# Optimization experiments

Hardware: AMD Instinct MI355X
Metric: run time of the kernel (lower is better)

## Reference

```python
import jax, jax.numpy as jnp
import numpy as np

DIM = 192
N_HEADS = 8
HEAD_DIM = DIM // N_HEADS
SCALE = 1.0 / np.sqrt(HEAD_DIM).astype(np.float32)
H_GRID, W_GRID = 32, 64
KH, KW = 7, 11


def build_local_mask():
    # Equivalent to the torch double-loop construction: token (h2,w2) may attend
    # to (h,w) iff |h2-h| <= KH//2 and |w2-w| <= KW//2 (odd kernels).
    hh = jnp.arange(H_GRID)
    ww = jnp.arange(W_GRID)
    dh_ok = jnp.abs(hh[:, None] - hh[None, :]) <= KH // 2  # [H, H]
    dw_ok = jnp.abs(ww[:, None] - ww[None, :]) <= KW // 2  # [W, W]
    allowed = dh_ok[:, None, :, None] & dw_ok[None, :, None, :]  # [H, W, H, W]
    allowed = allowed.reshape(H_GRID * W_GRID, H_GRID * W_GRID)
    return jnp.where(allowed, 0.0, -jnp.inf).astype(jnp.float32)  # [N, N]


def setup_inputs() -> dict:
    key = jax.random.key(0)
    ks = jax.random.split(key, 5)
    B, N = 4, H_GRID * W_GRID
    w_std = 1.0 / np.sqrt(DIM)
    x = jax.random.normal(ks[0], (B, N, DIM), dtype=jnp.float32)
    qkv_w = jax.random.normal(ks[1], (3 * DIM, DIM), dtype=jnp.float32) * w_std
    qkv_b = jax.random.normal(ks[2], (3 * DIM,), dtype=jnp.float32) * 0.02
    proj_w = jax.random.normal(ks[3], (DIM, DIM), dtype=jnp.float32) * w_std
    proj_b = jax.random.normal(ks[4], (DIM,), dtype=jnp.float32) * 0.02
    mask = build_local_mask()
    return {"x": x, "qkv_w": qkv_w, "qkv_b": qkv_b,
            "proj_w": proj_w, "proj_b": proj_b, "mask": mask}


def reference(x, qkv_w, qkv_b, proj_w, proj_b, mask):
    B, N, _ = x.shape
    qkv = x @ qkv_w.T + qkv_b                              # [B, N, 3*DIM]
    qkv = qkv.reshape(B, N, 3, N_HEADS, HEAD_DIM)
    qkv = jnp.transpose(qkv, (2, 0, 3, 1, 4))              # [3, B, h, N, d]
    q, k, v = qkv[0] * SCALE, qkv[1], qkv[2]
    attn = jnp.einsum('bhnd,bhmd->bhnm', q, k) + mask      # [B, h, N, N]
    attn = jax.nn.softmax(attn, axis=-1)                   # == log_softmax().exp()
    out = jnp.einsum('bhnm,bhmd->bhnd', attn, v)           # [B, h, N, d]
    out = jnp.transpose(out, (0, 2, 1, 3)).reshape(B, N, DIM)
    return out @ proj_w.T + proj_b
```

## Files before the change

### kernel.cpp

```cpp
#include <hip/hip_runtime.h>
#include <math.h>

#define H_GRID 32
#define W_GRID 64
#define NTOK   2048
#define NHEADS 8
#define HD     24
#define DIMC   192
#define BATCH  4

static constexpr float SCALE = 0.20412414523193154f;

typedef unsigned short ushort;
typedef unsigned int   uint;
typedef __attribute__((ext_vector_type(8))) _Float16 f16x8;
typedef __attribute__((ext_vector_type(4))) float    f32x4;

static __device__ __forceinline__ float4 ld4(const float* p) { return *(const float4*)p; }

static __device__ __forceinline__ ushort f2h(float f) {
    _Float16 h = (_Float16)f;
    union { _Float16 h; ushort u; } c; c.h = h; return c.u;
}
static __device__ __forceinline__ float h2f(ushort u) {
    union { ushort u; _Float16 h; } c; c.u = u; return (float)c.h;
}
static __device__ __forceinline__ f16x8 cvt8(float4 a, float4 b) {
    f16x8 r;
    r[0] = (_Float16)a.x; r[1] = (_Float16)a.y; r[2] = (_Float16)a.z; r[3] = (_Float16)a.w;
    r[4] = (_Float16)b.x; r[5] = (_Float16)b.y; r[6] = (_Float16)b.z; r[7] = (_Float16)b.w;
    return r;
}

__global__ __launch_bounds__(256, 4) void gemm_qkv(const float* __restrict__ x,
                                                   const float* __restrict__ Wf,
                                                   const float* __restrict__ bias,
                                                   ushort* __restrict__ Qh,
                                                   ushort* __restrict__ Kh,
                                                   ushort* __restrict__ VTh) {
    __shared__ ushort Ws[64 * 200];

    const int t    = threadIdx.x;
    const int wave = t >> 6, lane = t & 63;
    const int bx   = blockIdx.x;
    const int by   = blockIdx.y;
    const int m0   = bx * 64 + wave * 16;
    const int j0   = by * 64;
    const int n16  = lane & 15;
    const int kq   = lane >> 4;

    for (int i = t; i < 1536; i += 256) {
        const int r = i / 24, c = i - (i / 24) * 24;
        const float* wsrc = &Wf[(size_t)(j0 + r) * 192 + c * 8];
        const float4 w0 = ld4(wsrc), w1 = ld4(wsrc + 4);
        *(ushort4*)&Ws[r * 200 + c * 8] =
            make_ushort4(f2h(w0.x), f2h(w0.y), f2h(w0.z), f2h(w0.w));
        *(ushort4*)&Ws[r * 200 + c * 8 + 4] =
            make_ushort4(f2h(w1.x), f2h(w1.y), f2h(w1.z), f2h(w1.w));
    }

    if (by == 0) {
        for (int i = t; i < 1024; i += 256) {
            const int tok = bx * 64 + (i >> 4);
            const int h_  = (i >> 1) & 7;
            ushort* dst = (i & 1) ? Kh : Qh;
            const uint4 z = {0u, 0u, 0u, 0u};
            *(uint4*)&dst[((size_t)((tok >> 11) * 8 + h_) * 2048 + (tok & 2047)) * 32 + 24] = z;
        }
    }

    const float* ap = x + (size_t)(m0 + n16) * 192 + kq * 8;
    f16x8 af[6];
#pragma unroll
    for (int ks = 0; ks < 6; ks++) {
        const float4 a0 = ld4(ap + ks * 32);
        const float4 a1 = ld4(ap + ks * 32 + 4);
        af[ks] = cvt8(a0, a1);
    }

    f32x4 acc[4] = {f32x4{0,0,0,0}, f32x4{0,0,0,0}, f32x4{0,0,0,0}, f32x4{0,0,0,0}};

    __syncthreads();

#pragma unroll
    for (int ks = 0; ks < 6; ks++) {
#pragma unroll
        for (int nt = 0; nt < 4; nt++) {
            const f16x8 bf = *(const f16x8*)&Ws[(nt * 16 + n16) * 200 + kq * 8 + ks * 32];
            acc[nt] = __builtin_amdgcn_mfma_f32_16x16x32_f16(af[ks], bf, acc[nt], 0, 0, 0);
        }
    }

    const int band  = by / 3;
    const int mrow0 = m0 + kq * 4;
    const int b_    = mrow0 >> 11;
    const int tok0  = mrow0 & 2047;

    if (band == 2) {
#pragma unroll
        for (int nt = 0; nt < 4; nt++) {
            const int col = j0 + nt * 16 + n16;
            const int lc  = col - 384;
            const int h_  = lc / 24;
            const int d_  = lc - h_ * 24;
            const float bv = bias[col];
            ushort vv[4];
#pragma unroll
            for (int r = 0; r < 4; r++) vv[r] = f2h(acc[nt][r] + bv);
            const size_t addr = ((size_t)(b_ * 8 + h_) * 32 + d_) * 2080 + 8 + tok0;
            *(ushort4*)&VTh[addr] = make_ushort4(vv[0], vv[1], vv[2], vv[3]);
        }
    } else {
        const float sc_ = band ? 1.0f : SCALE;
        __syncthreads();
#pragma unroll
        for (int nt = 0; nt < 4; nt++) {
            const int col = j0 + nt * 16 + n16;
            const float bv = bias[col];
#pragma unroll
            for (int r = 0; r < 4; r++) {
                Ws[(wave * 16 + kq * 4 + r) * 68 + nt * 16 + n16] =
                    f2h((acc[nt][r] + bv) * sc_);
            }
        }
        __syncthreads();
        ushort* dst = band ? Kh : Qh;
        const int lc0 = j0 - band * 192;
#pragma unroll
        for (int it = 0; it < 4; it++) {
            const int item = t + 256 * it;
            const int tokl = item >> 4;
            const int cg   = item & 15;
            const ushort4 v = *(const ushort4*)&Ws[tokl * 68 + cg * 4];
            const int lc = lc0 + cg * 4;
            const int h_ = lc / 24;
            const int d0 = lc - h_ * 24;
            const int m  = bx * 64 + tokl;
            const size_t addr = ((size_t)((m >> 11) * 8 + h_) * 2048 + (m & 2047)) * 32 + d0;
            *(ushort4*)&dst[addr] = v;
        }
    }
}

__global__ __launch_bounds__(256, 4) void attn_mfma(const ushort* __restrict__ Qh,
                                                    const ushort* __restrict__ Kh,
                                                    const ushort* __restrict__ VTh,
                                                    ushort* __restrict__ aws) {
    const int id    = blockIdx.x;
    const int head  = id & 7;
    const int qtile = (id >> 3) & 63;
    const int b     = id >> 9;
    const int qh0   = (qtile >> 3) * 4;
    const int qw0   = (qtile & 7) * 8;
    const int kw0a  = qw0 - 8;

    const int t = threadIdx.x;
    const int w = t >> 6, lane = t & 63;
    const int n16 = lane & 15, quad = lane >> 4;
    const int bh = b * 8 + head;

    __shared__ ushort P[32 * 328];
    __shared__ ushort Os[32 * 28];
    __shared__ float  mxbuf[64], sumbuf[64];

    const ushort* Qb = Qh + (size_t)bh * 65536;
    const ushort* Kb = Kh + (size_t)bh * 65536;

    const int mt = w >> 1, nth = w & 1;
    const int mrow = 16 * mt + n16;
    const int tq_a = ((qh0 + (mrow >> 3)) << 6) + qw0 + (mrow & 7);
    const f16x8 qf = *(const f16x8*)&Qb[(size_t)tq_a * 32 + quad * 8];

    float sv[10][4];
    float mx4[4] = {-3e38f, -3e38f, -3e38f, -3e38f};
#pragma unroll
    for (int half = 0; half < 2; half++) {
        f16x8 kf[5];
        int khvv[5], kwvv[5];
#pragma unroll
        for (int jj = 0; jj < 5; jj++) {
            const int j = half * 5 + jj;
            const int slot = (nth * 10 + j) * 16 + n16;
            const int rr = slot >> 5, cc = slot & 31;
            khvv[jj] = qh0 - 3 + rr;
            kwvv[jj] = kw0a + cc;
            const int tok = (min(max(khvv[jj], 0), 31) << 6) + min(max(kwvv[jj], 0), 63);
            kf[jj] = *(const f16x8*)&Kb[(size_t)tok * 32 + quad * 8];
        }
#pragma unroll
        for (int jj = 0; jj < 5; jj++) {
            const int j = half * 5 + jj;
            f32x4 a = f32x4{0, 0, 0, 0};
            a = __builtin_amdgcn_mfma_f32_16x16x32_f16(qf, kf[jj], a, 0, 0, 0);
            const int khv = khvv[jj], kwv = kwvv[jj];
            const bool kok = (khv >= 0) && (khv < 32) && (kwv >= 0) && (kwv < 64);
#pragma unroll
            for (int r = 0; r < 4; r++) {
                const int m   = 16 * mt + quad * 4 + r;
                const int qhv = qh0 + (m >> 3);
                const int qwv = qw0 + (m & 7);
                const bool valid = kok && (abs(khv - qhv) <= 3) && (abs(kwv - qwv) <= 5);
                const float s = valid ? a[r] : -3e38f;
                sv[j][r] = s;
                mx4[r] = fmaxf(mx4[r], s);
            }
        }
    }
#pragma unroll
    for (int d = 1; d < 16; d <<= 1)
#pragma unroll
        for (int r = 0; r < 4; r++) mx4[r] = fmaxf(mx4[r], __shfl_xor(mx4[r], d));
    if (n16 == 0) {
#pragma unroll
        for (int r = 0; r < 4; r++) mxbuf[w * 16 + quad * 4 + r] = mx4[r];
    }
    __syncthreads();
#pragma unroll
    for (int r = 0; r < 4; r++) mx4[r] = fmaxf(mx4[r], mxbuf[(w ^ 1) * 16 + quad * 4 + r]);

    float sum4[4] = {0.f, 0.f, 0.f, 0.f};
#pragma unroll
    for (int j = 0; j < 10; j++) {
        const int slot = (nth * 10 + j) * 16 + n16;
#pragma unroll
        for (int r = 0; r < 4; r++) {
            const float p = __expf(sv[j][r] - mx4[r]);
            const ushort ph = f2h(p);
            sum4[r] += h2f(ph);
            P[(16 * mt + quad * 4 + r) * 328 + slot] = ph;
        }
    }
#pragma unroll
    for (int d = 1; d < 16; d <<= 1)
#pragma unroll
        for (int r = 0; r < 4; r++) sum4[r] += __shfl_xor(sum4[r], d);
    if (n16 == 0) {
#pragma unroll
        for (int r = 0; r < 4; r++) sumbuf[w * 16 + quad * 4 + r] = sum4[r];
    }
    __syncthreads();

    const int mtP = w >> 1, ntP = w & 1;
    const int dcol = 16 * ntP + n16;
    const ushort* VTb = VTh + (size_t)bh * 66560;
    f32x4 acc = f32x4{0, 0, 0, 0};
#pragma unroll
    for (int half = 0; half < 2; half++) {
        f16x8 vf[5], pa[5];
#pragma unroll
        for (int kk = 0; kk < 5; kk++) {
            const int ks = half * 5 + kk;
            const int kh_cl = min(max(qh0 - 3 + ks, 0), 31);
            vf[kk] = *(const f16x8*)&VTb[(size_t)dcol * 2080 + 8 + (kh_cl << 6) + kw0a + quad * 8];
            pa[kk] = *(const f16x8*)&P[(16 * mtP + n16) * 328 + ks * 32 + quad * 8];
        }
#pragma unroll
        for (int kk = 0; kk < 5; kk++) {
            acc = __builtin_amdgcn_mfma_f32_16x16x32_f16(pa[kk], vf[kk], acc, 0, 0, 0);
        }
    }
    if (dcol < 24) {
#pragma unroll
        for (int r = 0; r < 4; r++) {
            const int m = 16 * mtP + quad * 4 + r;
            const float tot = sumbuf[(2 * mtP) * 16 + (m & 15)] +
                              sumbuf[(2 * mtP + 1) * 16 + (m & 15)];
            Os[m * 28 + dcol] = f2h(acc[r] / tot);
        }
    }
    __syncthreads();

    if (t < 192) {
        const int tok = t / 6, g = t - (t / 6) * 6;
        const ushort4 v = *(const ushort4*)&Os[tok * 28 + g * 4];
        const int tq = ((qh0 + (tok >> 3)) << 6) + qw0 + (tok & 7);
        *(ushort4*)&aws[((size_t)(b * 2048 + tq)) * 192 + head * 24 + g * 4] = v;
    }
}

__global__ __launch_bounds__(128, 4) void gemm_proj(const ushort* __restrict__ Ah,
                                                    const float* __restrict__ Wf,
                                                    const float* __restrict__ bias,
                                                    float* __restrict__ C) {
    __shared__ ushort Ws[64 * 200];

    const int t    = threadIdx.x;
    const int wave = t >> 6, lane = t & 63;
    const int m0   = blockIdx.x * 32 + wave * 16;
    const int j0   = blockIdx.y * 64;
    const int n16  = lane & 15;
    const int kq   = lane >> 4;

    for (int i = t; i < 1536; i += 128) {
        const int r = i / 24, c = i - (i / 24) * 24;
        const float* wsrc = &Wf[(size_t)(j0 + r) * 192 + c * 8];
        const float4 w0 = ld4(wsrc), w1 = ld4(wsrc + 4);
        *(ushort4*)&Ws[r * 200 + c * 8] =
            make_ushort4(f2h(w0.x), f2h(w0.y), f2h(w0.z), f2h(w0.w));
        *(ushort4*)&Ws[r * 200 + c * 8 + 4] =
            make_ushort4(f2h(w1.x), f2h(w1.y), f2h(w1.z), f2h(w1.w));
    }

    const ushort* ap = Ah + (size_t)(m0 + n16) * 192 + kq * 8;

    f16x8 af[6];
#pragma unroll
    for (int ks = 0; ks < 6; ks++) af[ks] = *(const f16x8*)(ap + ks * 32);

    f32x4 acc[4] = {f32x4{0,0,0,0}, f32x4{0,0,0,0}, f32x4{0,0,0,0}, f32x4{0,0,0,0}};

    __syncthreads();

#pragma unroll
    for (int ks = 0; ks < 6; ks++) {
#pragma unroll
        for (int nt = 0; nt < 4; nt++) {
            const f16x8 bf = *(const f16x8*)&Ws[(nt * 16 + n16) * 200 + kq * 8 + ks * 32];
            acc[nt] = __builtin_amdgcn_mfma_f32_16x16x32_f16(af[ks], bf, acc[nt], 0, 0, 0);
        }
    }

#pragma unroll
    for (int nt = 0; nt < 4; nt++) {
        const int col = j0 + nt * 16 + n16;
        const float bv = bias[col];
#pragma unroll
        for (int r = 0; r < 4; r++) {
            const int m = m0 + kq * 4 + r;
            C[(size_t)m * 192 + col] = acc[nt][r] + bv;
        }
    }
}

extern "C" void kernel_launch(void* const* d_in, const int* in_sizes, int n_in,
                              void* d_out, int out_size, void* d_ws, size_t ws_size,
                              hipStream_t stream) {
    const float* x      = (const float*)d_in[0];
    const float* qkv_w  = (const float*)d_in[1];
    const float* qkv_b  = (const float*)d_in[2];
    const float* proj_w = (const float*)d_in[3];
    const float* proj_b = (const float*)d_in[4];

    char* wsb = (char*)d_ws;
    ushort* Qh   = (ushort*)(wsb + 0);
    ushort* Kh   = (ushort*)(wsb + 4194304);
    ushort* VTh  = (ushort*)(wsb + 8388608);
    ushort* awsh = (ushort*)(wsb + 12648448);
    float*  out  = (float*)d_out;

    hipLaunchKernelGGL(gemm_qkv, dim3(128, 9), dim3(256), 0, stream,
                       x, qkv_w, qkv_b, Qh, Kh, VTh);
    hipLaunchKernelGGL(attn_mfma, dim3(2048), dim3(256), 0, stream,
                       Qh, Kh, VTh, awsh);
    hipLaunchKernelGGL(gemm_proj, dim3(256, 3), dim3(128), 0, stream,
                       awsh, proj_w, proj_b, out);
}
```

Baseline: 110.5 us.

## Fuse QKV, attention and projection into one persistent kernel with grid barriers

New measurement: 349.3 us. 3.16x slower.

```diff
diff --git a/kernel.cpp b/kernel.cpp
--- a/kernel.cpp
+++ b/kernel.cpp
@@ -9,6 +9,8 @@
 #define DIMC   192
 #define BATCH  4
 
+#define NBLK   1024u
+
 static constexpr float SCALE = 0.20412414523193154f;
 
 typedef unsigned short ushort;
@@ -32,302 +34,334 @@
     return r;
 }
 
-__global__ __launch_bounds__(256, 4) void gemm_qkv(const float* __restrict__ x,
-                                                   const float* __restrict__ Wf,
-                                                   const float* __restrict__ bias,
-                                                   ushort* __restrict__ Qh,
-                                                   ushort* __restrict__ Kh,
-                                                   ushort* __restrict__ VTh) {
-    __shared__ ushort Ws[64 * 200];
-
-    const int t    = threadIdx.x;
-    const int wave = t >> 6, lane = t & 63;
-    const int bx   = blockIdx.x;
-    const int by   = blockIdx.y;
-    const int m0   = bx * 64 + wave * 16;
-    const int j0   = by * 64;
-    const int n16  = lane & 15;
-    const int kq   = lane >> 4;
-
-    for (int i = t; i < 1536; i += 256) {
-        const int r = i / 24, c = i - (i / 24) * 24;
-        const float* wsrc = &Wf[(size_t)(j0 + r) * 192 + c * 8];
-        const float4 w0 = ld4(wsrc), w1 = ld4(wsrc + 4);
-        *(ushort4*)&Ws[r * 200 + c * 8] =
-            make_ushort4(f2h(w0.x), f2h(w0.y), f2h(w0.z), f2h(w0.w));
-        *(ushort4*)&Ws[r * 200 + c * 8 + 4] =
-            make_ushort4(f2h(w1.x), f2h(w1.y), f2h(w1.z), f2h(w1.w));
+static __device__ __forceinline__ void gbar(uint* cnt) {
+    __syncthreads();
+    if (threadIdx.x == 0) {
+        __threadfence();
+        atomicAdd(cnt, 1u);
+        int spins = 0;
+        while (__hip_atomic_load(cnt, __ATOMIC_RELAXED, __HIP_MEMORY_SCOPE_AGENT) < NBLK) {
+            __builtin_amdgcn_s_sleep(8);
+            if (++spins > 50000000) break;
+        }
+        __threadfence();
     }
-
-    if (by == 0) {
-        for (int i = t; i < 1024; i += 256) {
-            const int tok = bx * 64 + (i >> 4);
-            const int h_  = (i >> 1) & 7;
-            ushort* dst = (i & 1) ? Kh : Qh;
-            const uint4 z = {0u, 0u, 0u, 0u};
-            *(uint4*)&dst[((size_t)((tok >> 11) * 8 + h_) * 2048 + (tok & 2047)) * 32 + 24] = z;
+    __syncthreads();
+}
+
+__global__ __launch_bounds__(256, 4) void fused(const float* __restrict__ x,
+                                                const float* __restrict__ qkv_w,
+                                                const float* __restrict__ qkv_b,
+                                                const float* __restrict__ proj_w,
+                                                const float* __restrict__ proj_b,
+                                                ushort* __restrict__ Qh,
+                                                ushort* __restrict__ Kh,
+                                                ushort* __restrict__ VTh,
+                                                ushort* __restrict__ awsh,
+                                                float* __restrict__ out,
+                                                uint* __restrict__ bar) {
+    union SMem {
+        ushort Ws[64 * 200];
+        struct {
+            ushort P[32 * 328];
+            ushort Os[32 * 28];
+            float  mxbuf[64];
+            float  sumbuf[64];
+        } a;
+        char force_lds[40960];
+    };
+    __shared__ SMem sm;
+
+    const int blkid = blockIdx.x;
+    const int t     = threadIdx.x;
+    const int wave  = t >> 6, lane = t & 63;
+    const int n16   = lane & 15;
+    const int kq    = lane >> 4;
+
+    for (int vt = blkid; vt < 1152; vt += 1024) {
+        const int bx = vt & 127;
+        const int by = vt >> 7;
+        const int j0 = by * 64;
+        const int m0 = bx * 64 + wave * 16;
+
+        __syncthreads();
+
+        for (int i = t; i < 1536; i += 256) {
+            const int r = i / 24, c = i - (i / 24) * 24;
+            const float* wsrc = &qkv_w[(size_t)(j0 + r) * 192 + c * 8];
+            const float4 w0 = ld4(wsrc), w1 = ld4(wsrc + 4);
+            *(ushort4*)&sm.Ws[r * 200 + c * 8] =
+                make_ushort4(f2h(w0.x), f2h(w0.y), f2h(w0.z), f2h(w0.w));
+            *(ushort4*)&sm.Ws[r * 200 + c * 8 + 4] =
+                make_ushort4(f2h(w1.x), f2h(w1.y), f2h(w1.z), f2h(w1.w));
+        }
+
+        if (by == 0) {
+            for (int i = t; i < 1024; i += 256) {
+                const int tok = bx * 64 + (i >> 4);
+                const int h_  = (i >> 1) & 7;
+                ushort* dst = (i & 1) ? Kh : Qh;
+                const uint4 z = {0u, 0u, 0u, 0u};
+                *(uint4*)&dst[((size_t)((tok >> 11) * 8 + h_) * 2048 + (tok & 2047)) * 32 + 24] = z;
+            }
+        }
+
+        const float* ap = x + (size_t)(m0 + n16) * 192 + kq * 8;
+        f16x8 af[6];
+#pragma unroll
+        for (int ks = 0; ks < 6; ks++) {
+            const float4 a0 = ld4(ap + ks * 32);
+            const float4 a1 = ld4(ap + ks * 32 + 4);
+            af[ks] = cvt8(a0, a1);
+        }
+
+        f32x4 acc[4] = {f32x4{0,0,0,0}, f32x4{0,0,0,0}, f32x4{0,0,0,0}, f32x4{0,0,0,0}};
+
+        __syncthreads();
+
+#pragma unroll
+        for (int ks = 0; ks < 6; ks++) {
+#pragma unroll
+            for (int nt = 0; nt < 4; nt++) {
+                const f16x8 bf = *(const f16x8*)&sm.Ws[(nt * 16 + n16) * 200 + kq * 8 + ks * 32];
+                acc[nt] = __builtin_amdgcn_mfma_f32_16x16x32_f16(af[ks], bf, acc[nt], 0, 0, 0);
+            }
+        }
+
+        const int band  = by / 3;
+        const int mrow0 = m0 + kq * 4;
+        const int b_    = mrow0 >> 11;
+        const int tok0  = mrow0 & 2047;
+
+        if (band == 2) {
+#pragma unroll
+            for (int nt = 0; nt < 4; nt++) {
+                const int col = j0 + nt * 16 + n16;
+                const int lc  = col - 384;
+                const int h_  = lc / 24;
+                const int d_  = lc - h_ * 24;
+                const float bv = qkv_b[col];
+                ushort vv[4];
+#pragma unroll
+                for (int r = 0; r < 4; r++) vv[r] = f2h(acc[nt][r] + bv);
+                const size_t addr = ((size_t)(b_ * 8 + h_) * 32 + d_) * 2080 + 8 + tok0;
+                *(ushort4*)&VTh[addr] = make_ushort4(vv[0], vv[1], vv[2], vv[3]);
+            }
+        } else {
+            const float sc_ = band ? 1.0f : SCALE;
+            __syncthreads();
+#pragma unroll
+            for (int nt = 0; nt < 4; nt++) {
+                const int col = j0 + nt * 16 + n16;
+                const float bv = qkv_b[col];
+#pragma unroll
+                for (int r = 0; r < 4; r++) {
+                    sm.Ws[(wave * 16 + kq * 4 + r) * 68 + nt * 16 + n16] =
+                        f2h((acc[nt][r] + bv) * sc_);
+                }
+            }
+            __syncthreads();
+            ushort* dst = band ? Kh : Qh;
+            const int lc0 = j0 - band * 192;
+#pragma unroll
+            for (int it = 0; it < 4; it++) {
+                const int item = t + 256 * it;
+                const int tokl = item >> 4;
+                const int cg   = item & 15;
+                const ushort4 v = *(const ushort4*)&sm.Ws[tokl * 68 + cg * 4];
+                const int lc = lc0 + cg * 4;
+                const int h_ = lc / 24;
+                const int d0 = lc - h_ * 24;
+                const int m  = bx * 64 + tokl;
+                const size_t addr = ((size_t)((m >> 11) * 8 + h_) * 2048 + (m & 2047)) * 32 + d0;
+                *(ushort4*)&dst[addr] = v;
+            }
         }
     }
 
-    const float* ap = x + (size_t)(m0 + n16) * 192 + kq * 8;
-    f16x8 af[6];
-#pragma unroll
-    for (int ks = 0; ks < 6; ks++) {
-        const float4 a0 = ld4(ap + ks * 32);
-        const float4 a1 = ld4(ap + ks * 32 + 4);
-        af[ks] = cvt8(a0, a1);
+    gbar(&bar[0]);
+
+    {
+        ushort* P      = sm.a.P;
+        ushort* Os     = sm.a.Os;
+        float*  mxbuf  = sm.a.mxbuf;
+        float*  sumbuf = sm.a.sumbuf;
+        const int w    = wave;
+        const int quad = kq;
+
+        for (int vb = blkid; vb < 2048; vb += 1024) {
+            __syncthreads();
+
+            const int head  = vb & 7;
+            const int qtile = (vb >> 3) & 63;
+            const int b     = vb >> 9;
+            const int qh0   = (qtile >> 3) * 4;
+            const int qw0   = (qtile & 7) * 8;
+            const int kw0a  = qw0 - 8;
+            const int bh    = b * 8 + head;
+
+            const ushort* Qb = Qh + (size_t)bh * 65536;
+            const ushort* Kb = Kh + (size_t)bh * 65536;
+
+            const int mt = w >> 1, nth = w & 1;
+            const int mrow = 16 * mt + n16;
+            const int tq_a = ((qh0 + (mrow >> 3)) << 6) + qw0 + (mrow & 7);
+            const f16x8 qf = *(const f16x8*)&Qb[(size_t)tq_a * 32 + quad * 8];
+
+            float sv[10][4];
+            float mx4[4] = {-3e38f, -3e38f, -3e38f, -3e38f};
+#pragma unroll
+            for (int half = 0; half < 2; half++) {
+                f16x8 kf[5];
+                int khvv[5], kwvv[5];
+#pragma unroll
+                for (int jj = 0; jj < 5; jj++) {
+                    const int j = half * 5 + jj;
+                    const int slot = (nth * 10 + j) * 16 + n16;
+                    const int rr = slot >> 5, cc = slot & 31;
+                    khvv[jj] = qh0 - 3 + rr;
+                    kwvv[jj] = kw0a + cc;
+                    const int tok = (min(max(khvv[jj], 0), 31) << 6) + min(max(kwvv[jj], 0), 63);
+                    kf[jj] = *(const f16x8*)&Kb[(size_t)tok * 32 + quad * 8];
+                }
+#pragma unroll
+                for (int jj = 0; jj < 5; jj++) {
+                    const int j = half * 5 + jj;
+                    f32x4 a = f32x4{0, 0, 0, 0};
+                    a = __builtin_amdgcn_mfma_f32_16x16x32_f16(qf, kf[jj], a, 0, 0, 0);
+                    const int khv = khvv[jj], kwv = kwvv[jj];
+                    const bool kok = (khv >= 0) && (khv < 32) && (kwv >= 0) && (kwv < 64);
+#pragma unroll
+                    for (int r = 0; r < 4; r++) {
+                        const int m   = 16 * mt + quad * 4 + r;
+                        const int qhv = qh0 + (m >> 3);
+                        const int qwv = qw0 + (m & 7);
+                        const bool valid = kok && (abs(khv - qhv) <= 3) && (abs(kwv - qwv) <= 5);
+                        const float s = valid ? a[r] : -3e38f;
+                        sv[j][r] = s;
+                        mx4[r] = fmaxf(mx4[r], s);
+                    }
+                }
+            }
+#pragma unroll
+            for (int d = 1; d < 16; d <<= 1)
+#pragma unroll
+                for (int r = 0; r < 4; r++) mx4[r] = fmaxf(mx4[r], __shfl_xor(mx4[r], d));
+            if (n16 == 0) {
+#pragma unroll
+                for (int r = 0; r < 4; r++) mxbuf[w * 16 + quad * 4 + r] = mx4[r];
+            }
+            __syncthreads();
+#pragma unroll
+            for (int r = 0; r < 4; r++) mx4[r] = fmaxf(mx4[r], mxbuf[(w ^ 1) * 16 + quad * 4 + r]);
+
+            float sum4[4] = {0.f, 0.f, 0.f, 0.f};
+#pragma unroll
+            for (int j = 0; j < 10; j++) {
+                const int slot = (nth * 10 + j) * 16 + n16;
+#pragma unroll
+                for (int r = 0; r < 4; r++) {
+                    const float p = __expf(sv[j][r] - mx4[r]);
+                    const ushort ph = f2h(p);
+                    sum4[r] += h2f(ph);
+                    P[(16 * mt + quad * 4 + r) * 328 + slot] = ph;
+                }
+            }
+#pragma unroll
+            for (int d = 1; d < 16; d <<= 1)
+#pragma unroll
+                for (int r = 0; r < 4; r++) sum4[r] += __shfl_xor(sum4[r], d);
+            if (n16 == 0) {
+#pragma unroll
+                for (int r = 0; r < 4; r++) sumbuf[w * 16 + quad * 4 + r] = sum4[r];
+            }
+            __syncthreads();
+
+            const int mtP = w >> 1, ntP = w & 1;
+            const int dcol = 16 * ntP + n16;
+            const ushort* VTb = VTh + (size_t)bh * 66560;
+            f32x4 acc = f32x4{0, 0, 0, 0};
+#pragma unroll
+            for (int half = 0; half < 2; half++) {
+                f16x8 vf[5], pa[5];
+#pragma unroll
+                for (int kk = 0; kk < 5; kk++) {
+                    const int ks = half * 5 + kk;
+                    const int kh_cl = min(max(qh0 - 3 + ks, 0), 31);
+                    vf[kk] = *(const f16x8*)&VTb[(size_t)dcol * 2080 + 8 + (kh_cl << 6) + kw0a + quad * 8];
+                    pa[kk] = *(const f16x8*)&P[(16 * mtP + n16) * 328 + ks * 32 + quad * 8];
+                }
+#pragma unroll
+                for (int kk = 0; kk < 5; kk++) {
+                    acc = __builtin_amdgcn_mfma_f32_16x16x32_f16(pa[kk], vf[kk], acc, 0, 0, 0);
+                }
+            }
+            if (dcol < 24) {
+#pragma unroll
+                for (int r = 0; r < 4; r++) {
+                    const int m = 16 * mtP + quad * 4 + r;
+                    const float tot = sumbuf[(2 * mtP) * 16 + (m & 15)] +
+                                      sumbuf[(2 * mtP + 1) * 16 + (m & 15)];
+                    Os[m * 28 + dcol] = f2h(acc[r] / tot);
+                }
+            }
+            __syncthreads();
+
+            if (t < 192) {
+                const int tok = t / 6, g = t - (t / 6) * 6;
+                const ushort4 v = *(const ushort4*)&Os[tok * 28 + g * 4];
+                const int tq = ((qh0 + (tok >> 3)) << 6) + qw0 + (tok & 7);
+                *(ushort4*)&awsh[((size_t)(b * 2048 + tq)) * 192 + head * 24 + g * 4] = v;
+            }
+        }
     }
 
-    f32x4 acc[4] = {f32x4{0,0,0,0}, f32x4{0,0,0,0}, f32x4{0,0,0,0}, f32x4{0,0,0,0}};
-
-    __syncthreads();
-
-#pragma unroll
-    for (int ks = 0; ks < 6; ks++) {
-#pragma unroll
-        for (int nt = 0; nt < 4; nt++) {
-            const f16x8 bf = *(const f16x8*)&Ws[(nt * 16 + n16) * 200 + kq * 8 + ks * 32];
-            acc[nt] = __builtin_amdgcn_mfma_f32_16x16x32_f16(af[ks], bf, acc[nt], 0, 0, 0);
-        }
-    }
-
-    const int band  = by / 3;
-    const int mrow0 = m0 + kq * 4;
-    const int b_    = mrow0 >> 11;
-    const int tok0  = mrow0 & 2047;
-
-    if (band == 2) {
+    gbar(&bar[16]);
+
+    if (blkid < 384) {
+        const int bx = blkid & 127;
+        const int by = blkid >> 7;
+        const int j0 = by * 64;
+        const int m0 = bx * 64 + wave * 16;
+
+        for (int i = t; i < 1536; i += 256) {
+            const int r = i / 24, c = i - (i / 24) * 24;
+            const float* wsrc = &proj_w[(size_t)(j0 + r) * 192 + c * 8];
+            const float4 w0 = ld4(wsrc), w1 = ld4(wsrc + 4);
+            *(ushort4*)&sm.Ws[r * 200 + c * 8] =
+                make_ushort4(f2h(w0.x), f2h(w0.y), f2h(w0.z), f2h(w0.w));
+            *(ushort4*)&sm.Ws[r * 200 + c * 8 + 4] =
+                make_ushort4(f2h(w1.x), f2h(w1.y), f2h(w1.z), f2h(w1.w));
+        }
+
+        const ushort* ap = awsh + (size_t)(m0 + n16) * 192 + kq * 8;
+
+        f16x8 af[6];
+#pragma unroll
+        for (int ks = 0; ks < 6; ks++) af[ks] = *(const f16x8*)(ap + ks * 32);
+
+        f32x4 acc[4] = {f32x4{0,0,0,0}, f32x4{0,0,0,0}, f32x4{0,0,0,0}, f32x4{0,0,0,0}};
+
+        __syncthreads();
+
+#pragma unroll
+        for (int ks = 0; ks < 6; ks++) {
+#pragma unroll
+            for (int nt = 0; nt < 4; nt++) {
+                const f16x8 bf = *(const f16x8*)&sm.Ws[(nt * 16 + n16) * 200 + kq * 8 + ks * 32];
+                acc[nt] = __builtin_amdgcn_mfma_f32_16x16x32_f16(af[ks], bf, acc[nt], 0, 0, 0);
+            }
+        }
+
 #pragma unroll
         for (int nt = 0; nt < 4; nt++) {
             const int col = j0 + nt * 16 + n16;
-            const int lc  = col - 384;
-            const int h_  = lc / 24;
-            const int d_  = lc - h_ * 24;
-            const float bv = bias[col];
-            ushort vv[4];
-#pragma unroll
-            for (int r = 0; r < 4; r++) vv[r] = f2h(acc[nt][r] + bv);
-            const size_t addr = ((size_t)(b_ * 8 + h_) * 32 + d_) * 2080 + 8 + tok0;
-            *(ushort4*)&VTh[addr] = make_ushort4(vv[0], vv[1], vv[2], vv[3]);
-        }
-    } else {
-        const float sc_ = band ? 1.0f : SCALE;
-        __syncthreads();
-#pragma unroll
-        for (int nt = 0; nt < 4; nt++) {
-            const int col = j0 + nt * 16 + n16;
-            const float bv = bias[col];
+            const float bv = proj_b[col];
 #pragma unroll
             for (int r = 0; r < 4; r++) {
-                Ws[(wave * 16 + kq * 4 + r) * 68 + nt * 16 + n16] =
-                    f2h((acc[nt][r] + bv) * sc_);
-            }
-        }
-        __syncthreads();
-        ushort* dst = band ? Kh : Qh;
-        const int lc0 = j0 - band * 192;
-#pragma unroll
-        for (int it = 0; it < 4; it++) {
-            const int item = t + 256 * it;
-            const int tokl = item >> 4;
-            const int cg   = item & 15;
-            const ushort4 v = *(const ushort4*)&Ws[tokl * 68 + cg * 4];
-            const int lc = lc0 + cg * 4;
-            const int h_ = lc / 24;
-            const int d0 = lc - h_ * 24;
-            const int m  = bx * 64 + tokl;
-            const size_t addr = ((size_t)((m >> 11) * 8 + h_) * 2048 + (m & 2047)) * 32 + d0;
-            *(ushort4*)&dst[addr] = v;
-        }
-    }
-}
-
-__global__ __launch_bounds__(256, 4) void attn_mfma(const ushort* __restrict__ Qh,
-                                                    const ushort* __restrict__ Kh,
-                                                    const ushort* __restrict__ VTh,
-                                                    ushort* __restrict__ aws) {
-    const int id    = blockIdx.x;
-    const int head  = id & 7;
-    const int qtile = (id >> 3) & 63;
-    const int b     = id >> 9;
-    const int qh0   = (qtile >> 3) * 4;
-    const int qw0   = (qtile & 7) * 8;
-    const int kw0a  = qw0 - 8;
-
-    const int t = threadIdx.x;
-    const int w = t >> 6, lane = t & 63;
-    const int n16 = lane & 15, quad = lane >> 4;
-    const int bh = b * 8 + head;
-
-    __shared__ ushort P[32 * 328];
-    __shared__ ushort Os[32 * 28];
-    __shared__ float  mxbuf[64], sumbuf[64];
-
-    const ushort* Qb = Qh + (size_t)bh * 65536;
-    const ushort* Kb = Kh + (size_t)bh * 65536;
-
-    const int mt = w >> 1, nth = w & 1;
-    const int mrow = 16 * mt + n16;
-    const int tq_a = ((qh0 + (mrow >> 3)) << 6) + qw0 + (mrow & 7);
-    const f16x8 qf = *(const f16x8*)&Qb[(size_t)tq_a * 32 + quad * 8];
-
-    float sv[10][4];
-    float mx4[4] = {-3e38f, -3e38f, -3e38f, -3e38f};
-#pragma unroll
-    for (int half = 0; half < 2; half++) {
-        f16x8 kf[5];
-        int khvv[5], kwvv[5];
-#pragma unroll
-        for (int jj = 0; jj < 5; jj++) {
-            const int j = half * 5 + jj;
-            const int slot = (nth * 10 + j) * 16 + n16;
-            const int rr = slot >> 5, cc = slot & 31;
-            khvv[jj] = qh0 - 3 + rr;
-            kwvv[jj] = kw0a + cc;
-            const int tok = (min(max(khvv[jj], 0), 31) << 6) + min(max(kwvv[jj], 0), 63);
-            kf[jj] = *(const f16x8*)&Kb[(size_t)tok * 32 + quad * 8];
-        }
-#pragma unroll
-        for (int jj = 0; jj < 5; jj++) {
-            const int j = half * 5 + jj;
-            f32x4 a = f32x4{0, 0, 0, 0};
-            a = __builtin_amdgcn_mfma_f32_16x16x32_f16(qf, kf[jj], a, 0, 0, 0);
-            const int khv = khvv[jj], kwv = kwvv[jj];
-            const bool kok = (khv >= 0) && (khv < 32) && (kwv >= 0) && (kwv < 64);
-#pragma unroll
-            for (int r = 0; r < 4; r++) {
-                const int m   = 16 * mt + quad * 4 + r;
-                const int qhv = qh0 + (m >> 3);
-                const int qwv = qw0 + (m & 7);
-                const bool valid = kok && (abs(khv - qhv) <= 3) && (abs(kwv - qwv) <= 5);
-                const float s = valid ? a[r] : -3e38f;
-                sv[j][r] = s;
-                mx4[r] = fmaxf(mx4[r], s);
-            }
-        }
-    }
-#pragma unroll
-    for (int d = 1; d < 16; d <<= 1)
-#pragma unroll
-        for (int r = 0; r < 4; r++) mx4[r] = fmaxf(mx4[r], __shfl_xor(mx4[r], d));
-    if (n16 == 0) {
-#pragma unroll
-        for (int r = 0; r < 4; r++) mxbuf[w * 16 + quad * 4 + r] = mx4[r];
-    }
-    __syncthreads();
-#pragma unroll
-    for (int r = 0; r < 4; r++) mx4[r] = fmaxf(mx4[r], mxbuf[(w ^ 1) * 16 + quad * 4 + r]);
-
-    float sum4[4] = {0.f, 0.f, 0.f, 0.f};
-#pragma unroll
-    for (int j = 0; j < 10; j++) {
-        const int slot = (nth * 10 + j) * 16 + n16;
-#pragma unroll
-        for (int r = 0; r < 4; r++) {
-            const float p = __expf(sv[j][r] - mx4[r]);
-            const ushort ph = f2h(p);
-            sum4[r] += h2f(ph);
-            P[(16 * mt + quad * 4 + r) * 328 + slot] = ph;
-        }
-    }
-#pragma unroll
-    for (int d = 1; d < 16; d <<= 1)
-#pragma unroll
-        for (int r = 0; r < 4; r++) sum4[r] += __shfl_xor(sum4[r], d);
-    if (n16 == 0) {
-#pragma unroll
-        for (int r = 0; r < 4; r++) sumbuf[w * 16 + quad * 4 + r] = sum4[r];
-    }
-    __syncthreads();
-
-    const int mtP = w >> 1, ntP = w & 1;
-    const int dcol = 16 * ntP + n16;
-    const ushort* VTb = VTh + (size_t)bh * 66560;
-    f32x4 acc = f32x4{0, 0, 0, 0};
-#pragma unroll
-    for (int half = 0; half < 2; half++) {
-        f16x8 vf[5], pa[5];
-#pragma unroll
-        for (int kk = 0; kk < 5; kk++) {
-            const int ks = half * 5 + kk;
-            const int kh_cl = min(max(qh0 - 3 + ks, 0), 31);
-            vf[kk] = *(const f16x8*)&VTb[(size_t)dcol * 2080 + 8 + (kh_cl << 6) + kw0a + quad * 8];
-            pa[kk] = *(const f16x8*)&P[(16 * mtP + n16) * 328 + ks * 32 + quad * 8];
-        }
-#pragma unroll
-        for (int kk = 0; kk < 5; kk++) {
-            acc = __builtin_amdgcn_mfma_f32_16x16x32_f16(pa[kk], vf[kk], acc, 0, 0, 0);
-        }
-    }
-    if (dcol < 24) {
-#pragma unroll
-        for (int r = 0; r < 4; r++) {
-            const int m = 16 * mtP + quad * 4 + r;
-            const float tot = sumbuf[(2 * mtP) * 16 + (m & 15)] +
-                              sumbuf[(2 * mtP + 1) * 16 + (m & 15)];
-            Os[m * 28 + dcol] = f2h(acc[r] / tot);
-        }
-    }
-    __syncthreads();
-
-    if (t < 192) {
-        const int tok = t / 6, g = t - (t / 6) * 6;
-        const ushort4 v = *(const ushort4*)&Os[tok * 28 + g * 4];
-        const int tq = ((qh0 + (tok >> 3)) << 6) + qw0 + (tok & 7);
-        *(ushort4*)&aws[((size_t)(b * 2048 + tq)) * 192 + head * 24 + g * 4] = v;
-    }
-}
-
-__global__ __launch_bounds__(128, 4) void gemm_proj(const ushort* __restrict__ Ah,
-                                                    const float* __restrict__ Wf,
-                                                    const float* __restrict__ bias,
-                                                    float* __restrict__ C) {
-    __shared__ ushort Ws[64 * 200];
-
-    const int t    = threadIdx.x;
-    const int wave = t >> 6, lane = t & 63;
-    const int m0   = blockIdx.x * 32 + wave * 16;
-    const int j0   = blockIdx.y * 64;
-    const int n16  = lane & 15;
-    const int kq   = lane >> 4;
-
-    for (int i = t; i < 1536; i += 128) {
-        const int r = i / 24, c = i - (i / 24) * 24;
-        const float* wsrc = &Wf[(size_t)(j0 + r) * 192 + c * 8];
-        const float4 w0 = ld4(wsrc), w1 = ld4(wsrc + 4);
-        *(ushort4*)&Ws[r * 200 + c * 8] =
-            make_ushort4(f2h(w0.x), f2h(w0.y), f2h(w0.z), f2h(w0.w));
-        *(ushort4*)&Ws[r * 200 + c * 8 + 4] =
-            make_ushort4(f2h(w1.x), f2h(w1.y), f2h(w1.z), f2h(w1.w));
-    }
-
-    const ushort* ap = Ah + (size_t)(m0 + n16) * 192 + kq * 8;
-
-    f16x8 af[6];
-#pragma unroll
-    for (int ks = 0; ks < 6; ks++) af[ks] = *(const f16x8*)(ap + ks * 32);
-
-    f32x4 acc[4] = {f32x4{0,0,0,0}, f32x4{0,0,0,0}, f32x4{0,0,0,0}, f32x4{0,0,0,0}};
-
-    __syncthreads();
-
-#pragma unroll
-    for (int ks = 0; ks < 6; ks++) {
-#pragma unroll
-        for (int nt = 0; nt < 4; nt++) {
-            const f16x8 bf = *(const f16x8*)&Ws[(nt * 16 + n16) * 200 + kq * 8 + ks * 32];
-            acc[nt] = __builtin_amdgcn_mfma_f32_16x16x32_f16(af[ks], bf, acc[nt], 0, 0, 0);
-        }
-    }
-
-#pragma unroll
-    for (int nt = 0; nt < 4; nt++) {
-        const int col = j0 + nt * 16 + n16;
-        const float bv = bias[col];
-#pragma unroll
-        for (int r = 0; r < 4; r++) {
-            const int m = m0 + kq * 4 + r;
-            C[(size_t)m * 192 + col] = acc[nt][r] + bv;
+                const int m = m0 + kq * 4 + r;
+                out[(size_t)m * 192 + col] = acc[nt][r] + bv;
+            }
         }
     }
 }
@@ -346,12 +380,10 @@
     ushort* Kh   = (ushort*)(wsb + 4194304);
     ushort* VTh  = (ushort*)(wsb + 8388608);
     ushort* awsh = (ushort*)(wsb + 12648448);
+    uint*   bar  = (uint*)(wsb + 16777216);
     float*  out  = (float*)d_out;
 
-    hipLaunchKernelGGL(gemm_qkv, dim3(128, 9), dim3(256), 0, stream,
-                       x, qkv_w, qkv_b, Qh, Kh, VTh);
-    hipLaunchKernelGGL(attn_mfma, dim3(2048), dim3(256), 0, stream,
-                       Qh, Kh, VTh, awsh);
-    hipLaunchKernelGGL(gemm_proj, dim3(256, 3), dim3(128), 0, stream,
-                       awsh, proj_w, proj_b, out);
-}
+    hipMemsetAsync(bar, 0, 128, stream);
+    hipLaunchKernelGGL(fused, dim3(1024), dim3(256), 0, stream,
+                       x, qkv_w, qkv_b, proj_w, proj_b, Qh, Kh, VTh, awsh, out, bar);
+}
```
